# Kernel optimization log

Hardware: AMD Instinct MI355X
Metric: run time of the kernel (lower is better)

## Reference

```python
import jax, jax.numpy as jnp
import numpy as np

LN_EPS = 1e-5


def setup_inputs() -> dict:
    key = jax.random.key(0)
    ks = jax.random.split(key, 8)
    b, c, h, w = 16, 1024, 64, 64
    r = 64  # max(c // 16, 16)
    return {
        "x": jax.random.normal(ks[0], (b, c, h, w), dtype=jnp.float32),
        "wm": jax.random.normal(ks[1], (c,), dtype=jnp.float32) * 0.02,
        "bm": jax.random.normal(ks[2], (1,), dtype=jnp.float32) * 0.02,
        "w1": jax.random.normal(ks[3], (r, c), dtype=jnp.float32) * 0.02,
        "b1": jax.random.normal(ks[4], (r,), dtype=jnp.float32) * 0.02,
        "ln_g": jnp.ones((r,), dtype=jnp.float32),
        "ln_b": jnp.zeros((r,), dtype=jnp.float32),
        "w2": jax.random.normal(ks[5], (c, r), dtype=jnp.float32) * 0.02,
        "b2": jax.random.normal(ks[6], (c,), dtype=jnp.float32) * 0.02,
    }


def reference(x, wm, bm, w1, b1, ln_g, ln_b, w2, b2):
    b, c, h, w = x.shape
    s = h * w
    xf = x.reshape(b, c, s)  # [b, c, hw]
    # 1x1 conv mask: Conv2d(c -> 1)
    cm = jnp.einsum("bcs,c->bs", xf, wm) + bm  # [b, hw]
    unary = jax.nn.softmax(cm, axis=-1)  # softmax over spatial dim (dim=2 of [b,1,hw])
    # 'spatial' whitening: subtract mean over dim 1 (size 1) -> identically zero mask
    cm_w = cm - cm  # faithful to context_mask -= context_mask.mean(1).unsqueeze(1)
    mask = jax.nn.softmax(cm_w, axis=-1) + unary  # uniform 1/hw + unary
    # pooling: matmul(input_x [b,1,c,hw], mask [b,1,hw,1]) -> [b, c]
    context = jnp.einsum("bcs,bs->bc", xf, mask)
    # transform MLP: 1x1 conv -> LayerNorm([r,1,1]) -> ReLU -> 1x1 conv
    t = context @ w1.T + b1  # [b, r]
    mu = jnp.mean(t, axis=-1, keepdims=True)
    var = jnp.mean(jnp.square(t - mu), axis=-1, keepdims=True)
    t = (t - mu) * jax.lax.rsqrt(var + LN_EPS) * ln_g + ln_b
    t = jax.nn.relu(t)
    out = t @ w2.T + b2  # [b, c]
    return out.reshape(b, c, 1, 1)
```

## Files before the change

### kernel.cpp

```cpp
#include <hip/hip_runtime.h>
#include <hip/hip_bf16.h>

#define B 16
#define C 1024
#define S 4096
#define R 64
#define NCCHUNK 16
#define NSCHUNK 4

typedef float f4 __attribute__((ext_vector_type(4)));

__global__ __launch_bounds__(256) void k1_cm_partial(
    const float* __restrict__ x, const float* __restrict__ wm,
    float* __restrict__ cm_part) {
  int bid = blockIdx.x;
  int cchunk = bid & (NCCHUNK - 1);
  int schunk = (bid >> 4) & (NSCHUNK - 1);
  int b = bid >> 6;
  int s0 = schunk * 256 + threadIdx.x;
  const f4* xp = (const f4*)x + ((size_t)b * C + (size_t)cchunk * 64) * (S / 4) + s0;
  const float* wp = wm + cchunk * 64;
  f4 a0 = {0.f, 0.f, 0.f, 0.f}, a1 = {0.f, 0.f, 0.f, 0.f};
#pragma unroll 8
  for (int c = 0; c < 64; c += 2) {
    f4 v0 = __builtin_nontemporal_load(xp + (size_t)c * (S / 4));
    f4 v1 = __builtin_nontemporal_load(xp + (size_t)(c + 1) * (S / 4));
    a0 += wp[c] * v0;
    a1 += wp[c + 1] * v1;
  }
  ((f4*)cm_part)[((size_t)cchunk * B + b) * (S / 4) + s0] = a0 + a1;
}

__global__ __launch_bounds__(256) void k2_softmax(
    const float* __restrict__ cm_part, float* __restrict__ e,
    float* __restrict__ zinv) {
  int b = blockIdx.x, tid = threadIdx.x;
  f4 v[4] = {{0.f,0.f,0.f,0.f},{0.f,0.f,0.f,0.f},{0.f,0.f,0.f,0.f},{0.f,0.f,0.f,0.f}};
#pragma unroll
  for (int k = 0; k < NCCHUNK; ++k) {
    const f4* cp = (const f4*)cm_part + ((size_t)k * B + b) * (S / 4);
#pragma unroll
    for (int j = 0; j < 4; ++j) v[j] += cp[tid + j * 256];
  }
  float m = -1e30f;
#pragma unroll
  for (int j = 0; j < 4; ++j)
    m = fmaxf(m, fmaxf(fmaxf(v[j][0], v[j][1]), fmaxf(v[j][2], v[j][3])));
  for (int off = 32; off > 0; off >>= 1) m = fmaxf(m, __shfl_xor(m, off));
  __shared__ float redm[4], redz[4];
  int wid = tid >> 6, lane = tid & 63;
  if (lane == 0) redm[wid] = m;
  __syncthreads();
  m = fmaxf(fmaxf(redm[0], redm[1]), fmaxf(redm[2], redm[3]));
  float zs = 0.f;
  f4 ev[4];
#pragma unroll
  for (int j = 0; j < 4; ++j) {
#pragma unroll
    for (int q = 0; q < 4; ++q) {
      float t = expf(v[j][q] - m);
      ev[j][q] = t;
      zs += t;
    }
  }
  for (int off = 32; off > 0; off >>= 1) zs += __shfl_xor(zs, off);
  if (lane == 0) redz[wid] = zs;
  __syncthreads();
  zs = redz[0] + redz[1] + redz[2] + redz[3];
  f4* ep = (f4*)(e + (size_t)b * S);
#pragma unroll
  for (int j = 0; j < 4; ++j) ep[tid + j * 256] = ev[j];
  if (tid == 0) zinv[b] = 1.0f / zs;
}

__global__ __launch_bounds__(256) void k3_context(
    const float* __restrict__ x, const float* __restrict__ e,
    const float* __restrict__ zinv, float* __restrict__ context) {
  int row = blockIdx.x * 4 + (threadIdx.x >> 6);
  int lane = threadIdx.x & 63;
  int b = row >> 10;
  const f4* xp = (const f4*)(x + (size_t)row * S);
  const f4* ep = (const f4*)(e + (size_t)b * S);
  float zi = zinv[b];
  f4 s1 = {0.f, 0.f, 0.f, 0.f}, s2 = {0.f, 0.f, 0.f, 0.f};
#pragma unroll
  for (int i = 0; i < 16; ++i) {
    f4 xv = __builtin_nontemporal_load(xp + lane + i * 64);
    f4 evv = ep[lane + i * 64];
    s1 += xv;
    s2 += xv * evv;
  }
  float tot = (s1[0] + s1[1] + s1[2] + s1[3]) * (1.0f / S) +
              (s2[0] + s2[1] + s2[2] + s2[3]) * zi;
  for (int off = 32; off > 0; off >>= 1) tot += __shfl_down(tot, off);
  if (lane == 0) context[row] = tot;
}

__global__ __launch_bounds__(256) void k4_mlp(
    const float* __restrict__ context, const float* __restrict__ w1,
    const float* __restrict__ b1, const float* __restrict__ ln_g,
    const float* __restrict__ ln_b, const float* __restrict__ w2,
    const float* __restrict__ b2, float* __restrict__ out) {
  int b = blockIdx.x;
  int tid = threadIdx.x, wid = tid >> 6, lane = tid & 63;
  __shared__ float tt[R];
  const f4* ctxp = (const f4*)(context + (size_t)b * C);
  f4 c0 = ctxp[lane], c1 = ctxp[lane + 64], c2 = ctxp[lane + 128], c3 = ctxp[lane + 192];
#pragma unroll
  for (int i = 0; i < 16; ++i) {
    int r = wid * 16 + i;
    const f4* wp = (const f4*)(w1 + (size_t)r * C);
    f4 p = c0 * wp[lane] + c1 * wp[lane + 64] + c2 * wp[lane + 128] + c3 * wp[lane + 192];
    float dot = p[0] + p[1] + p[2] + p[3];
#pragma unroll
    for (int off = 32; off > 0; off >>= 1) dot += __shfl_xor(dot, off);
    if (lane == 0) tt[r] = dot + b1[r];
  }
  __syncthreads();
  if (tid < 64) {
    float v = tt[tid];
    float mu = v;
    for (int off = 1; off < 64; off <<= 1) mu += __shfl_xor(mu, off);
    mu *= (1.0f / R);
    float d = v - mu;
    float var = d * d;
    for (int off = 1; off < 64; off <<= 1) var += __shfl_xor(var, off);
    var *= (1.0f / R);
    tt[tid] = fmaxf(d * rsqrtf(var + 1e-5f) * ln_g[tid] + ln_b[tid], 0.0f);
  }
  __syncthreads();
  f4 t4[16];
#pragma unroll
  for (int k = 0; k < 16; ++k) t4[k] = *(const f4*)(tt + k * 4);
#pragma unroll
  for (int cc = 0; cc < 4; ++cc) {
    int c = tid + cc * 256;
    const f4* w2p = (const f4*)(w2 + (size_t)c * R);
    f4 acc = {0.f, 0.f, 0.f, 0.f};
#pragma unroll
    for (int k = 0; k < 16; ++k) acc += w2p[k] * t4[k];
    out[(size_t)b * C + c] = acc[0] + acc[1] + acc[2] + acc[3] + b2[c];
  }
}

extern "C" void kernel_launch(void* const* d_in, const int* in_sizes, int n_in,
                              void* d_out, int out_size, void* d_ws, size_t ws_size,
                              hipStream_t stream) {
  const float* x    = (const float*)d_in[0];
  const float* wm   = (const float*)d_in[1];
  const float* w1   = (const float*)d_in[3];
  const float* b1   = (const float*)d_in[4];
  const float* ln_g = (const float*)d_in[5];
  const float* ln_b = (const float*)d_in[6];
  const float* w2   = (const float*)d_in[7];
  const float* b2   = (const float*)d_in[8];
  float* out = (float*)d_out;

  float* ws = (float*)d_ws;
  float* cm_part = ws;
  float* e       = cm_part + (size_t)NCCHUNK * B * S;
  float* zinv    = e + (size_t)B * S;
  float* context = zinv + 64;

  k1_cm_partial<<<B * NSCHUNK * NCCHUNK, 256, 0, stream>>>(x, wm, cm_part);
  k2_softmax<<<B, 256, 0, stream>>>(cm_part, e, zinv);
  k3_context<<<B * C / 4, 256, 0, stream>>>(x, e, zinv, context);
  k4_mlp<<<B, 256, 0, stream>>>(context, w1, b1, ln_g, ln_b, w2, b2, out);
}
```

Baseline: 417.2 us.

## Process batches in groups so x stays in last-level cache between passes

```diff
diff --git a/kernel.cpp b/kernel.cpp
--- a/kernel.cpp
+++ b/kernel.cpp
@@ -5,26 +5,26 @@
 #define C 1024
 #define S 4096
 #define R 64
-#define NCCHUNK 16
-#define NSCHUNK 4
+#define NCC 32
+#define BG 8
 
 typedef float f4 __attribute__((ext_vector_type(4)));
 
 __global__ __launch_bounds__(256) void k1_cm_partial(
     const float* __restrict__ x, const float* __restrict__ wm,
-    float* __restrict__ cm_part) {
+    float* __restrict__ cm_part, int b0) {
   int bid = blockIdx.x;
-  int cchunk = bid & (NCCHUNK - 1);
-  int schunk = (bid >> 4) & (NSCHUNK - 1);
-  int b = bid >> 6;
+  int cchunk = bid & (NCC - 1);
+  int schunk = (bid >> 5) & 3;
+  int b = b0 + (bid >> 7);
   int s0 = schunk * 256 + threadIdx.x;
-  const f4* xp = (const f4*)x + ((size_t)b * C + (size_t)cchunk * 64) * (S / 4) + s0;
-  const float* wp = wm + cchunk * 64;
+  const f4* xp = (const f4*)x + ((size_t)b * C + (size_t)cchunk * 32) * (S / 4) + s0;
+  const float* wp = wm + cchunk * 32;
   f4 a0 = {0.f, 0.f, 0.f, 0.f}, a1 = {0.f, 0.f, 0.f, 0.f};
 #pragma unroll 8
-  for (int c = 0; c < 64; c += 2) {
-    f4 v0 = __builtin_nontemporal_load(xp + (size_t)c * (S / 4));
-    f4 v1 = __builtin_nontemporal_load(xp + (size_t)(c + 1) * (S / 4));
+  for (int c = 0; c < 32; c += 2) {
+    f4 v0 = xp[(size_t)c * (S / 4)];
+    f4 v1 = xp[(size_t)(c + 1) * (S / 4)];
     a0 += wp[c] * v0;
     a1 += wp[c + 1] * v1;
   }
@@ -33,11 +33,11 @@
 
 __global__ __launch_bounds__(256) void k2_softmax(
     const float* __restrict__ cm_part, float* __restrict__ e,
-    float* __restrict__ zinv) {
-  int b = blockIdx.x, tid = threadIdx.x;
+    float* __restrict__ zinv, int b0) {
+  int b = b0 + blockIdx.x, tid = threadIdx.x;
   f4 v[4] = {{0.f,0.f,0.f,0.f},{0.f,0.f,0.f,0.f},{0.f,0.f,0.f,0.f},{0.f,0.f,0.f,0.f}};
 #pragma unroll
-  for (int k = 0; k < NCCHUNK; ++k) {
+  for (int k = 0; k < NCC; ++k) {
     const f4* cp = (const f4*)cm_part + ((size_t)k * B + b) * (S / 4);
 #pragma unroll
     for (int j = 0; j < 4; ++j) v[j] += cp[tid + j * 256];
@@ -75,8 +75,8 @@
 
 __global__ __launch_bounds__(256) void k3_context(
     const float* __restrict__ x, const float* __restrict__ e,
-    const float* __restrict__ zinv, float* __restrict__ context) {
-  int row = blockIdx.x * 4 + (threadIdx.x >> 6);
+    const float* __restrict__ zinv, float* __restrict__ context, int b0) {
+  int row = b0 * C + blockIdx.x * 4 + (threadIdx.x >> 6);
   int lane = threadIdx.x & 63;
   int b = row >> 10;
   const f4* xp = (const f4*)(x + (size_t)row * S);
@@ -85,7 +85,7 @@
   f4 s1 = {0.f, 0.f, 0.f, 0.f}, s2 = {0.f, 0.f, 0.f, 0.f};
 #pragma unroll
   for (int i = 0; i < 16; ++i) {
-    f4 xv = __builtin_nontemporal_load(xp + lane + i * 64);
+    f4 xv = xp[lane + i * 64];
     f4 evv = ep[lane + i * 64];
     s1 += xv;
     s2 += xv * evv;
@@ -158,12 +158,14 @@
 
   float* ws = (float*)d_ws;
   float* cm_part = ws;
-  float* e       = cm_part + (size_t)NCCHUNK * B * S;
+  float* e       = cm_part + (size_t)NCC * B * S;
   float* zinv    = e + (size_t)B * S;
   float* context = zinv + 64;
 
-  k1_cm_partial<<<B * NSCHUNK * NCCHUNK, 256, 0, stream>>>(x, wm, cm_part);
-  k2_softmax<<<B, 256, 0, stream>>>(cm_part, e, zinv);
-  k3_context<<<B * C / 4, 256, 0, stream>>>(x, e, zinv, context);
+  for (int b0 = 0; b0 < B; b0 += BG) {
+    k1_cm_partial<<<BG * NCC * 4, 256, 0, stream>>>(x, wm, cm_part, b0);
+    k2_softmax<<<BG, 256, 0, stream>>>(cm_part, e, zinv, b0);
+    k3_context<<<BG * C / 4, 256, 0, stream>>>(x, e, zinv, context, b0);
+  }
   k4_mlp<<<B, 256, 0, stream>>>(context, w1, b1, ln_g, ln_b, w2, b2, out);
 }
```

Result: slower. 457.1 us (+9.6%).

## Parallelize softmax with atomic partition sum and split MLP across more blocks

Applied to the files above, without the earlier changes.

```diff
diff --git a/kernel.cpp b/kernel.cpp
--- a/kernel.cpp
+++ b/kernel.cpp
@@ -12,7 +12,8 @@
 
 __global__ __launch_bounds__(256) void k1_cm_partial(
     const float* __restrict__ x, const float* __restrict__ wm,
-    float* __restrict__ cm_part) {
+    float* __restrict__ cm_part, float* __restrict__ zsum) {
+  if (blockIdx.x == 0 && threadIdx.x < B) zsum[threadIdx.x] = 0.0f;
   int bid = blockIdx.x;
   int cchunk = bid & (NCCHUNK - 1);
   int schunk = (bid >> 4) & (NSCHUNK - 1);
@@ -31,57 +32,36 @@
   ((f4*)cm_part)[((size_t)cchunk * B + b) * (S / 4) + s0] = a0 + a1;
 }
 
-__global__ __launch_bounds__(256) void k2_softmax(
+__global__ __launch_bounds__(256) void k2_expz(
     const float* __restrict__ cm_part, float* __restrict__ e,
-    float* __restrict__ zinv) {
-  int b = blockIdx.x, tid = threadIdx.x;
-  f4 v[4] = {{0.f,0.f,0.f,0.f},{0.f,0.f,0.f,0.f},{0.f,0.f,0.f,0.f},{0.f,0.f,0.f,0.f}};
+    float* __restrict__ zsum) {
+  int b = blockIdx.x >> 4, j = blockIdx.x & 15;
+  int s = j * 256 + threadIdx.x;
+  float acc = 0.f;
 #pragma unroll
-  for (int k = 0; k < NCCHUNK; ++k) {
-    const f4* cp = (const f4*)cm_part + ((size_t)k * B + b) * (S / 4);
-#pragma unroll
-    for (int j = 0; j < 4; ++j) v[j] += cp[tid + j * 256];
-  }
-  float m = -1e30f;
-#pragma unroll
-  for (int j = 0; j < 4; ++j)
-    m = fmaxf(m, fmaxf(fmaxf(v[j][0], v[j][1]), fmaxf(v[j][2], v[j][3])));
-  for (int off = 32; off > 0; off >>= 1) m = fmaxf(m, __shfl_xor(m, off));
-  __shared__ float redm[4], redz[4];
-  int wid = tid >> 6, lane = tid & 63;
-  if (lane == 0) redm[wid] = m;
+  for (int k = 0; k < NCCHUNK; ++k)
+    acc += cm_part[((size_t)k * B + b) * S + s];
+  float ev = __expf(acc);
+  e[(size_t)b * S + s] = ev;
+  float zs = ev;
+  for (int off = 32; off > 0; off >>= 1) zs += __shfl_xor(zs, off);
+  __shared__ float red[4];
+  int wid = threadIdx.x >> 6, lane = threadIdx.x & 63;
+  if (lane == 0) red[wid] = zs;
   __syncthreads();
-  m = fmaxf(fmaxf(redm[0], redm[1]), fmaxf(redm[2], redm[3]));
-  float zs = 0.f;
-  f4 ev[4];
-#pragma unroll
-  for (int j = 0; j < 4; ++j) {
-#pragma unroll
-    for (int q = 0; q < 4; ++q) {
-      float t = expf(v[j][q] - m);
-      ev[j][q] = t;
-      zs += t;
-    }
-  }
-  for (int off = 32; off > 0; off >>= 1) zs += __shfl_xor(zs, off);
-  if (lane == 0) redz[wid] = zs;
-  __syncthreads();
-  zs = redz[0] + redz[1] + redz[2] + redz[3];
-  f4* ep = (f4*)(e + (size_t)b * S);
-#pragma unroll
-  for (int j = 0; j < 4; ++j) ep[tid + j * 256] = ev[j];
-  if (tid == 0) zinv[b] = 1.0f / zs;
+  if (threadIdx.x == 0)
+    atomicAdd(zsum + b, red[0] + red[1] + red[2] + red[3]);
 }
 
 __global__ __launch_bounds__(256) void k3_context(
     const float* __restrict__ x, const float* __restrict__ e,
-    const float* __restrict__ zinv, float* __restrict__ context) {
+    const float* __restrict__ zsum, float* __restrict__ context) {
   int row = blockIdx.x * 4 + (threadIdx.x >> 6);
   int lane = threadIdx.x & 63;
   int b = row >> 10;
   const f4* xp = (const f4*)(x + (size_t)row * S);
   const f4* ep = (const f4*)(e + (size_t)b * S);
-  float zi = zinv[b];
+  float zi = 1.0f / zsum[b];
   f4 s1 = {0.f, 0.f, 0.f, 0.f}, s2 = {0.f, 0.f, 0.f, 0.f};
 #pragma unroll
   for (int i = 0; i < 16; ++i) {
@@ -96,51 +76,51 @@
   if (lane == 0) context[row] = tot;
 }
 
-__global__ __launch_bounds__(256) void k4_mlp(
+__global__ __launch_bounds__(256) void k4a_fc1(
     const float* __restrict__ context, const float* __restrict__ w1,
-    const float* __restrict__ b1, const float* __restrict__ ln_g,
-    const float* __restrict__ ln_b, const float* __restrict__ w2,
-    const float* __restrict__ b2, float* __restrict__ out) {
-  int b = blockIdx.x;
-  int tid = threadIdx.x, wid = tid >> 6, lane = tid & 63;
-  __shared__ float tt[R];
+    const float* __restrict__ b1, float* __restrict__ tt_g) {
+  int b = blockIdx.x >> 2, q = blockIdx.x & 3;
+  int wid = threadIdx.x >> 6, lane = threadIdx.x & 63;
   const f4* ctxp = (const f4*)(context + (size_t)b * C);
   f4 c0 = ctxp[lane], c1 = ctxp[lane + 64], c2 = ctxp[lane + 128], c3 = ctxp[lane + 192];
 #pragma unroll
-  for (int i = 0; i < 16; ++i) {
-    int r = wid * 16 + i;
+  for (int i = 0; i < 4; ++i) {
+    int r = q * 16 + wid * 4 + i;
     const f4* wp = (const f4*)(w1 + (size_t)r * C);
     f4 p = c0 * wp[lane] + c1 * wp[lane + 64] + c2 * wp[lane + 128] + c3 * wp[lane + 192];
     float dot = p[0] + p[1] + p[2] + p[3];
-#pragma unroll
     for (int off = 32; off > 0; off >>= 1) dot += __shfl_xor(dot, off);
-    if (lane == 0) tt[r] = dot + b1[r];
+    if (lane == 0) tt_g[b * R + r] = dot + b1[r];
   }
-  __syncthreads();
-  if (tid < 64) {
-    float v = tt[tid];
-    float mu = v;
-    for (int off = 1; off < 64; off <<= 1) mu += __shfl_xor(mu, off);
-    mu *= (1.0f / R);
-    float d = v - mu;
-    float var = d * d;
-    for (int off = 1; off < 64; off <<= 1) var += __shfl_xor(var, off);
-    var *= (1.0f / R);
-    tt[tid] = fmaxf(d * rsqrtf(var + 1e-5f) * ln_g[tid] + ln_b[tid], 0.0f);
-  }
+}
+
+__global__ __launch_bounds__(256) void k4b_ln_fc2(
+    const float* __restrict__ tt_g, const float* __restrict__ ln_g,
+    const float* __restrict__ ln_b, const float* __restrict__ w2,
+    const float* __restrict__ b2, float* __restrict__ out) {
+  int b = blockIdx.x >> 2, q = blockIdx.x & 3;
+  int tid = threadIdx.x, lane = tid & 63;
+  __shared__ float tts[R];
+  float v = tt_g[b * R + lane];
+  float mu = v;
+  for (int off = 1; off < 64; off <<= 1) mu += __shfl_xor(mu, off);
+  mu *= (1.0f / R);
+  float d = v - mu;
+  float var = d * d;
+  for (int off = 1; off < 64; off <<= 1) var += __shfl_xor(var, off);
+  var *= (1.0f / R);
+  float t = fmaxf(d * rsqrtf(var + 1e-5f) * ln_g[lane] + ln_b[lane], 0.0f);
+  if (tid < 64) tts[lane] = t;
   __syncthreads();
   f4 t4[16];
 #pragma unroll
-  for (int k = 0; k < 16; ++k) t4[k] = *(const f4*)(tt + k * 4);
+  for (int k = 0; k < 16; ++k) t4[k] = *(const f4*)(tts + k * 4);
+  int c = q * 256 + tid;
+  const f4* w2p = (const f4*)(w2 + (size_t)c * R);
+  f4 acc = {0.f, 0.f, 0.f, 0.f};
 #pragma unroll
-  for (int cc = 0; cc < 4; ++cc) {
-    int c = tid + cc * 256;
-    const f4* w2p = (const f4*)(w2 + (size_t)c * R);
-    f4 acc = {0.f, 0.f, 0.f, 0.f};
-#pragma unroll
-    for (int k = 0; k < 16; ++k) acc += w2p[k] * t4[k];
-    out[(size_t)b * C + c] = acc[0] + acc[1] + acc[2] + acc[3] + b2[c];
-  }
+  for (int k = 0; k < 16; ++k) acc += w2p[k] * t4[k];
+  out[(size_t)b * C + c] = acc[0] + acc[1] + acc[2] + acc[3] + b2[c];
 }
 
 extern "C" void kernel_launch(void* const* d_in, const int* in_sizes, int n_in,
@@ -159,11 +139,13 @@
   float* ws = (float*)d_ws;
   float* cm_part = ws;
   float* e       = cm_part + (size_t)NCCHUNK * B * S;
-  float* zinv    = e + (size_t)B * S;
-  float* context = zinv + 64;
+  float* zsum    = e + (size_t)B * S;
+  float* tt_g    = zsum + 64;
+  float* context = tt_g + (size_t)B * R;
 
-  k1_cm_partial<<<B * NSCHUNK * NCCHUNK, 256, 0, stream>>>(x, wm, cm_part);
-  k2_softmax<<<B, 256, 0, stream>>>(cm_part, e, zinv);
-  k3_context<<<B * C / 4, 256, 0, stream>>>(x, e, zinv, context);
-  k4_mlp<<<B, 256, 0, stream>>>(context, w1, b1, ln_g, ln_b, w2, b2, out);
+  k1_cm_partial<<<B * NSCHUNK * NCCHUNK, 256, 0, stream>>>(x, wm, cm_part, zsum);
+  k2_expz<<<B * 16, 256, 0, stream>>>(cm_part, e, zsum);
+  k3_context<<<B * C / 4, 256, 0, stream>>>(x, e, zsum, context);
+  k4a_fc1<<<B * 4, 256, 0, stream>>>(context, w1, b1, tt_g);
+  k4b_ln_fc2<<<B * 4, 256, 0, stream>>>(tt_g, ln_g, ln_b, w2, b2, out);
 }
```

Result: faster. 402.2 us (-3.6%).
